# Kernel optimization log

Measured on AMD Instinct MI355X. Metric: run time of the kernel, lower is better.

Reference implementation:

```python
import jax, jax.numpy as jnp
import numpy as np

SLOTS, PER, EGO_D, PAIR_D, TER_D, TOK, HEADS, HDIM, VEC_H = 5, 15, 32, 10, 81, 32, 4, 8, 2


def layer_norm(x, s, b, eps=1e-6):
    mu = jnp.mean(x, axis=-1, keepdims=True)
    var = jnp.mean(jnp.square(x - mu), axis=-1, keepdims=True)
    return (x - mu) * jax.lax.rsqrt(var + eps) * s + b


def zero_masked(x, mask):
    while mask.ndim < x.ndim:
        mask = mask[..., None]
    return jnp.where(mask, x, 0.0)


def masked_softmax(logits, mask, axis):
    mask = mask.astype(jnp.bool_)
    while mask.ndim < logits.ndim:
        mask = mask[..., None]
    neg_big = jnp.finfo(logits.dtype).min
    has_any = jnp.any(mask, axis=axis, keepdims=True)
    ml = jnp.where(mask, logits, neg_big)
    ml = jnp.where(has_any, ml, 0.0)
    w = jax.nn.softmax(ml, axis=axis)
    w = jnp.where(mask, w, 0.0)
    denom = jnp.sum(w, axis=axis, keepdims=True)
    return jnp.where(denom > 0, w / denom, 0.0)


def _forward(x, w_ego, b_ego, w_pair, b_pair, w_ter, b_ter, w_invtok, b_invtok,
             tx_ln1_s, tx_ln1_b, tx_wq, tx_bq, tx_wk, tx_bk, tx_wv, tx_bv, tx_wo, tx_bo,
             tx_ln2_s, tx_ln2_b, tx_w1, tx_b1, tx_w2, tx_b2,
             sp_ln_s, sp_ln_b, sp_w, sp_b, sp_log_temp,
             ap_wq, ap_bq, ap_wk, ap_bk, ap_we, ap_be,
             flat_w, flat_b,
             vr_wego, vr_bego, vr_ln_s, vr_ln_b, vr_wh, vr_bh, vr_wl, vr_bl,
             z_w1, z_b1, z_ln1_s, z_ln1_b, z_w2, z_b2, z_ln2_s, z_ln2_b):
    gelu = jax.nn.gelu  # tanh-approximate, matching flax nn.gelu
    x = x.astype(jnp.float32)
    B, N, D = x.shape
    ego = x[..., :EGO_D]
    nbr = x[..., EGO_D:EGO_D + SLOTS * PER].reshape(B, N, SLOTS, PER)
    pair = x[..., EGO_D + SLOTS * PER:EGO_D + SLOTS * PER + PAIR_D]
    ter = x[..., -TER_D:]
    r = nbr[..., 0:3]; u = nbr[..., 3:6]; att_rel = nbr[..., 6:9]
    fire = nbr[..., 9:10]; teamdiff = nbr[..., 10:11]; inv4 = nbr[..., 11:15]
    mask = jnp.any(jnp.abs(r) > 1e-06, axis=-1)  # (B,N,K)
    att_norm = jnp.linalg.norm(att_rel, axis=-1, keepdims=True)
    ego_e = gelu(ego @ w_ego + b_ego)
    pair_e = gelu(pair @ w_pair + b_pair)
    ter_e = gelu(ter @ w_ter + b_ter)
    inv = jnp.concatenate([fire, teamdiff, inv4, att_rel, att_norm], axis=-1)
    inv = zero_masked(inv, mask)
    inv_tok = zero_masked(gelu(inv @ w_invtok + b_invtok), mask)  # (B,N,K,TOK)
    # --- SetTxBlock ---
    has_any = jnp.any(mask, axis=-1, keepdims=True)  # (B,N,1)
    fallback = (jnp.arange(SLOTS) == 0)
    mask_safe = jnp.where(has_any, mask, fallback)
    amask = mask_safe[..., :, None] & mask_safe[..., None, :]  # (B,N,Kq,Kk)
    t = inv_tok
    y = layer_norm(t, tx_ln1_s, tx_ln1_b)
    q = (y @ tx_wq + tx_bq).reshape(B, N, SLOTS, HEADS, HDIM)
    k = (y @ tx_wk + tx_bk).reshape(B, N, SLOTS, HEADS, HDIM)
    v = (y @ tx_wv + tx_bv).reshape(B, N, SLOTS, HEADS, HDIM)
    scores = jnp.einsum('bnqhd,bnkhd->bnhqk', q, k) / jnp.sqrt(jnp.float32(HDIM))
    scores = jnp.where(amask[:, :, None, :, :], scores, jnp.finfo(scores.dtype).min)
    attn = jax.nn.softmax(scores, axis=-1)
    y = jnp.einsum('bnhqk,bnkhd->bnqhd', attn, v).reshape(B, N, SLOTS, TOK)
    y = zero_masked(y @ tx_wo + tx_bo, mask)
    t = t + y
    y = layer_norm(t, tx_ln2_s, tx_ln2_b)
    y = gelu(y @ tx_w1 + tx_b1) @ tx_w2 + tx_b2
    t = zero_masked(t + zero_masked(y, mask), mask)
    inv_tok = t
    # --- pools ---
    inv_sum = jnp.sum(inv_tok, axis=-2)
    inv_cnt = jnp.maximum(jnp.sum(mask, axis=-1, keepdims=True), 1)
    inv_mean = inv_sum / inv_cnt
    inv_max = jnp.max(jnp.where(mask[..., None], inv_tok, -1e9), axis=-2)
    inv_max = jnp.where(has_any, inv_max, 0.0)
    # MaskedSoftmaxPool
    yln = layer_norm(inv_tok, sp_ln_s, sp_ln_b)
    sc = (yln @ sp_w + sp_b)[..., 0]
    temp = jax.nn.softplus(sp_log_temp) + 0.001
    wts = masked_softmax(temp * sc, mask, axis=-1)
    inv_soft = jnp.sum(wts[..., None] * inv_tok, axis=-2)
    # EgoAdditivePool
    qe = (ego_e @ ap_wq + ap_bq)[:, :, None, :]
    ke = inv_tok @ ap_wk + ap_bk
    e = (jnp.tanh(qe + ke) @ ap_we + ap_be)[..., 0]
    alpha = masked_softmax(e, mask, axis=-1)
    inv_add = jnp.sum(alpha[..., None] * inv_tok, axis=-2)
    # flat readout
    inv_flat = 0.25 * gelu(inv_tok.reshape(B, N, SLOTS * TOK) @ flat_w + flat_b)
    # InvariantVectorReadout
    ego_h = jnp.broadcast_to((ego_e @ vr_wego + vr_bego)[:, :, None, :], (B, N, SLOTS, TOK))
    h = jnp.concatenate([layer_norm(inv_tok, vr_ln_s, vr_ln_b), ego_h], axis=-1)
    h = gelu(h @ vr_wh + vr_bh)
    logits = h @ vr_wl + vr_bl  # (B,N,K,VEC_H)
    alpha2 = masked_softmax(logits, mask, axis=-2)
    v_r = jnp.einsum('bnkh,bnkd->bnhd', alpha2, r).reshape(B, N, 3 * VEC_H)
    v_u = jnp.einsum('bnkh,bnkd->bnhd', alpha2, u).reshape(B, N, 3 * VEC_H)
    z = jnp.concatenate([ego_e, pair_e, ter_e, inv_mean, inv_max, inv_soft, inv_add, inv_flat, v_r, v_u], axis=-1)
    z = layer_norm(gelu(z @ z_w1 + z_b1), z_ln1_s, z_ln1_b)
    z = layer_norm(gelu(z @ z_w2 + z_b2), z_ln2_s, z_ln2_b)
    return z


def setup_inputs() -> dict:
    key = jax.random.key(0)
    ks = iter(jax.random.split(key, 40))
    B, N = 64, 2048
    ego = jax.random.normal(next(ks), (B, N, EGO_D), jnp.float32)
    nbr = jax.random.normal(next(ks), (B, N, SLOTS, PER), jnp.float32)
    keep = jax.random.bernoulli(next(ks), 0.7, (B, N, SLOTS))
    nbr = nbr * keep[..., None]  # zeroed slots -> masked out (r == 0)
    pair = jax.random.normal(next(ks), (B, N, PAIR_D), jnp.float32)
    ter = jax.random.normal(next(ks), (B, N, TER_D), jnp.float32)
    x = jnp.concatenate([ego, nbr.reshape(B, N, SLOTS * PER), pair, ter], axis=-1)
    def W(i, o, s=0.05):
        return jax.random.normal(next(ks), (i, o), jnp.float32) * s
    Z = lambda *sh: jnp.zeros(sh, jnp.float32)
    O = lambda *sh: jnp.ones(sh, jnp.float32)
    Z_DIM = 64 + 32 + 64 + 4 * TOK + 32 + 12  # 332
    return dict(
        x=x,
        w_ego=W(EGO_D, 64), b_ego=Z(64), w_pair=W(PAIR_D, 32), b_pair=Z(32),
        w_ter=W(TER_D, 64), b_ter=Z(64), w_invtok=W(10, TOK), b_invtok=Z(TOK),
        tx_ln1_s=O(TOK), tx_ln1_b=Z(TOK),
        tx_wq=W(TOK, TOK), tx_bq=Z(TOK), tx_wk=W(TOK, TOK), tx_bk=Z(TOK),
        tx_wv=W(TOK, TOK), tx_bv=Z(TOK), tx_wo=W(TOK, TOK), tx_bo=Z(TOK),
        tx_ln2_s=O(TOK), tx_ln2_b=Z(TOK),
        tx_w1=W(TOK, 2 * TOK), tx_b1=Z(2 * TOK), tx_w2=W(2 * TOK, TOK), tx_b2=Z(TOK),
        sp_ln_s=O(TOK), sp_ln_b=Z(TOK), sp_w=W(TOK, 1), sp_b=Z(1), sp_log_temp=jnp.float32(0.0),
        ap_wq=W(64, TOK), ap_bq=Z(TOK), ap_wk=W(TOK, TOK), ap_bk=Z(TOK), ap_we=W(TOK, 1), ap_be=Z(1),
        flat_w=W(SLOTS * TOK, 32), flat_b=Z(32),
        vr_wego=W(64, TOK), vr_bego=Z(TOK), vr_ln_s=O(TOK), vr_ln_b=Z(TOK),
        vr_wh=W(2 * TOK, TOK), vr_bh=Z(TOK), vr_wl=W(TOK, VEC_H), vr_bl=Z(VEC_H),
        z_w1=W(Z_DIM, 128), z_b1=Z(128), z_ln1_s=O(128), z_ln1_b=Z(128),
        z_w2=W(128, 128), z_b2=Z(128), z_ln2_s=O(128), z_ln2_b=Z(128),
    )


def reference(x, w_ego, b_ego, w_pair, b_pair, w_ter, b_ter, w_invtok, b_invtok,
              tx_ln1_s, tx_ln1_b, tx_wq, tx_bq, tx_wk, tx_bk, tx_wv, tx_bv, tx_wo, tx_bo,
              tx_ln2_s, tx_ln2_b, tx_w1, tx_b1, tx_w2, tx_b2,
              sp_ln_s, sp_ln_b, sp_w, sp_b, sp_log_temp,
              ap_wq, ap_bq, ap_wk, ap_bk, ap_we, ap_be,
              flat_w, flat_b,
              vr_wego, vr_bego, vr_ln_s, vr_ln_b, vr_wh, vr_bh, vr_wl, vr_bl,
              z_w1, z_b1, z_ln1_s, z_ln1_b, z_w2, z_b2, z_ln2_s, z_ln2_b):
    return _forward(x, w_ego, b_ego, w_pair, b_pair, w_ter, b_ter, w_invtok, b_invtok,
                    tx_ln1_s, tx_ln1_b, tx_wq, tx_bq, tx_wk, tx_bk, tx_wv, tx_bv, tx_wo, tx_bo,
                    tx_ln2_s, tx_ln2_b, tx_w1, tx_b1, tx_w2, tx_b2,
                    sp_ln_s, sp_ln_b, sp_w, sp_b, sp_log_temp,
                    ap_wq, ap_bq, ap_wk, ap_bk, ap_we, ap_be,
                    flat_w, flat_b,
                    vr_wego, vr_bego, vr_ln_s, vr_ln_b, vr_wh, vr_bh, vr_wl, vr_bl,
                    z_w1, z_b1, z_ln1_s, z_ln1_b, z_w2, z_b2, z_ln2_s, z_ln2_b)
```

## Files before the change

kernel.cpp:

```cpp
#include <hip/hip_runtime.h>
#include <hip/hip_bf16.h>

#define SLOTS 5
#define PER 15
#define EGO_DD 32
#define PAIR_DD 10
#define TER_DD 81
#define DX 198
#define ZDIM 332
#define NTOK (64*2048)
#define NEGB (-3.402823466e38f)
#define ST 36
#define HBST 68
#define YHS 40
#define HHS 72

#define T_EGO   0
#define T_PAIR  4
#define T_TER   6
#define T_INV   18
#define T_Q     20
#define T_K     22
#define T_V     24
#define T_O     26
// ... 39 lines not shown
  __hip_bfloat16 h = __float2bfloat16(x);
  return *reinterpret_cast<short*>(&h);
}
__device__ __forceinline__ float tanh_f(float x){
  float e = __expf(2.f*x);
  return 1.f - 2.f/(e+1.f);
}
__device__ __forceinline__ float gelu_f(float x){
  return 0.5f*x*(1.f+tanh_f(0.7978845608028654f*(x + 0.044715f*x*x*x)));
}
__device__ __forceinline__ s16x8 packrow(const float* r){
  s16x8 af;
  #pragma unroll
  for(int j=0;j<8;j++) af[j]=f2bf(r[j]);
  return af;
}
__device__ __forceinline__ s16x8 packrowb(const float* r, int k0, int K){
  s16x8 af;
  #pragma unroll
  for(int j=0;j<8;j++) af[j] = (k0+j<K) ? f2bf(r[k0+j]) : (short)0;
  return af;
}

__device__ void msm5(const float* lgv, const int* m, float* outp, float scale){
  bool any = m[0]||m[1]||m[2]||m[3]||m[4];
  if(!any){ for(int s2=0;s2<5;s2++) outp[s2]=0.f; return; }
  float mx=NEGB;
  for(int s2=0;s2<5;s2++) if(m[s2]) mx=fmaxf(mx, scale*lgv[s2]);
  float e[5], se=0.f;
  for(int s2=0;s2<5;s2++){ e[s2]= m[s2]? __expf(scale*lgv[s2]-mx):0.f; se+=e[s2]; }
  float inv=1.f/se;
  for(int s2=0;s2<5;s2++) outp[s2]=e[s2]*inv;
}

__device__ void ln5x32(const float* src, float* dst, const float* Sc, const float* Bi, int l){
  for (int sp=0; sp<6; sp+=2){
    int sl = sp + (l>>5), i = l&31;
    bool act = sl < SLOTS;
    float v = act ? src[sl*ST+i] : 0.f;
    float sum=v;
    sum+=__shfl_xor(sum,16,32); sum+=__shfl_xor(sum,8,32); sum+=__shfl_xor(sum,4,32);
    sum+=__shfl_xor(sum,2,32);  sum+=__shfl_xor(sum,1,32);
    float mu=sum*(1.f/32.f);
    float d = v-mu;
    float q=d*d;
    q+=__shfl_xor(q,16,32); q+=__shfl_xor(q,8,32); q+=__shfl_xor(q,4,32);
    q+=__shfl_xor(q,2,32);  q+=__shfl_xor(q,1,32);
    float rstd=rsqrtf(q*(1.f/32.f)+1e-6f);
    if(act) dst[sl*ST+i]=d*rstd*Sc[i]+Bi[i];
  }
}
__device__ void ln5x32h(const float* src, short* dst, const float* Sc, const float* Bi, int l){
  for (int sp=0; sp<6; sp+=2){
    int sl = sp + (l>>5), i = l&31;
    bool act = sl < SLOTS;
    float v = act ? src[sl*ST+i] : 0.f;
    float sum=v;
    sum+=__shfl_xor(sum,16,32); sum+=__shfl_xor(sum,8,32); sum+=__shfl_xor(sum,4,32);
    sum+=__shfl_xor(sum,2,32);  sum+=__shfl_xor(sum,1,32);
    float mu=sum*(1.f/32.f);
    float d = v-mu;
    float q=d*d;
    q+=__shfl_xor(q,16,32); q+=__shfl_xor(q,8,32); q+=__shfl_xor(q,4,32);
    q+=__shfl_xor(q,2,32);  q+=__shfl_xor(q,1,32);
    float rstd=rsqrtf(q*(1.f/32.f)+1e-6f);
    if(act) dst[sl*YHS+i]=f2bf(d*rstd*Sc[i]+Bi[i]);
  }
}

__global__ __launch_bounds__(256) void k_prep(P p, short* __restrict__ ws){
  int idx = blockIdx.x*256 + threadIdx.x;
  if (idx >= T_TOT*512) return;
  int j = idx & 7, lane = (idx>>3)&63, tile = idx>>9;
  const float* src; int K,N,ntc,t0;
  if      (tile < T_PAIR){ src=p.w_ego;   K=32;  N=64;  ntc=4; t0=T_EGO; }
  else if (tile < T_TER ){ src=p.w_pair;  K=10;  N=32;  ntc=2; t0=T_PAIR; }
  else if (tile < T_INV ){ src=p.w_ter;   K=81;  N=64;  ntc=4; t0=T_TER; }
  else if (tile < T_Q   ){ src=p.w_invtok;K=10;  N=32;  ntc=2; t0=T_INV; }
  else if (tile < T_K   ){ src=p.wq;      K=32;  N=32;  ntc=2; t0=T_Q; }
  else if (tile < T_V   ){ src=p.wk;      K=32;  N=32;  ntc=2; t0=T_K; }
  else if (tile < T_O   ){ src=p.wv;      K=32;  N=32;  ntc=2; t0=T_V; }
  else if (tile < T_W1  ){ src=p.wo;      K=32;  N=32;  ntc=2; t0=T_O; }
  else if (tile < T_W2  ){ src=p.w1;      K=32;  N=64;  ntc=4; t0=T_W1; }
  else if (tile < T_APQ ){ src=p.w2;      K=64;  N=32;  ntc=2; t0=T_W2; }
  else if (tile < T_APK ){ src=p.ap_wq;   K=64;  N=32;  ntc=2; t0=T_APQ; }
  else if (tile < T_FLAT){ src=p.ap_wk;   K=32;  N=32;  ntc=2; t0=T_APK; }
  else if (tile < T_VEGO){ src=p.flat_w;  K=160; N=32;  ntc=2; t0=T_FLAT; }
  else if (tile < T_VH  ){ src=p.vr_wego; K=64;  N=32;  ntc=2; t0=T_VEGO; }
  else if (tile < T_ZW1 ){ src=p.vr_wh;   K=64;  N=32;  ntc=2; t0=T_VH; }
  else if (tile < T_ZW2 ){ src=p.z_w1;    K=ZDIM;N=128; ntc=8; t0=T_ZW1; }
  else                   { src=p.z_w2;    K=128; N=128; ntc=8; t0=T_ZW2; }
  int tl = tile - t0, ktI = tl/ntc, ntI = tl%ntc;
  int k = ktI*32 + ((lane>>4)<<3) + j, n = ntI*16 + (lane&15);
  float v = (k<K && n<N) ? src[k*N+n] : 0.f;
  ws[idx] = f2bf(v);
}

#define WV 4
__global__ __launch_bounds__(256) void k_token(P p, float* __restrict__ outp,
                                               const short* __restrict__ wsb) {
  __shared__ __align__(16) float pool[WV*PW];
  __shared__ int mkA[WV][5];
  __shared__ int mksA[WV][5];
  const s16x8* wsv = (const s16x8*)wsb;
  int wid = threadIdx.x >> 6, l = threadIdx.x & 63;
  float* W   = pool + wid*PW;
  float* ego = W + OF_EGO;
  float* tv  = W + OF_TV;
  float* yb  = W + OF_YB;
  short* ybh = (short*)(W + OF_YB);
  float* U   = W + OF_U;
  float* at  = W + OF_AT;
  float* zb  = W + OF_ZB;
  float* qeb = W + OF_QEB;
  float* egh = W + OF_EGH;
  float* ru  = W + OF_RU;
  float* sm  = W + OF_SM;
  float* scs = sm+0; float* wts = sm+5; float* alp = sm+10; float* lg = sm+16; float* a2 = sm+26;
  int* mk  = mkA[wid];
  int* mks = mksA[wid];
  float* xb = U;
  float* qb = U;  float* kb = U+180;  float* vb = U+360;
  float* hb = U;
  short* hbh = (short*)(U + 344);
  float* vq = U;
  long tok = (long)blockIdx.x*WV + wid;
  int m = l & 15, q = l >> 4;
  int mm = m < 5 ? m : 4;
#define BFR(tile) wsv[(tile)*64 + l]

  {
    const float2* xr2 = (const float2*)(p.x + (size_t)tok*DX);
    float2* xb2 = (float2*)xb;
    for (int i=l;i<99;i+=64) xb2[i] = xr2[i];
  }
  WF();

  if (l < SLOTS) { int nb = EGO_DD + l*PER;
    mk[l] = (fabsf(xb[nb])>1e-6f || fabsf(xb[nb+1])>1e-6f || fabsf(xb[nb+2])>1e-6f) ? 1 : 0; }
  if (l < 30){ int sl=l/6, d=l%6; ru[l] = xb[EGO_DD + sl*PER + d]; }
  WF();
  int nmask = mk[0]+mk[1]+mk[2]+mk[3]+mk[4];
  bool hasany = nmask>0;
  if (l < SLOTS) mks[l] = hasany ? mk[l] : (l==0 ? 1 : 0);

  {
    s16x8 aE = packrow(&xb[q*8]);
    s16x8 aP = packrowb(&xb[107], q*8, 10);
    f32x4 e0={0,0,0,0},e1={0,0,0,0},e2={0,0,0,0},e3={0,0,0,0};
    e0=MFMA(aE,BFR(T_EGO+0),e0); e1=MFMA(aE,BFR(T_EGO+1),e1);
    e2=MFMA(aE,BFR(T_EGO+2),e2); e3=MFMA(aE,BFR(T_EGO+3),e3);
    f32x4 p0={0,0,0,0},p1={0,0,0,0};
    p0=MFMA(aP,BFR(T_PAIR+0),p0); p1=MFMA(aP,BFR(T_PAIR+1),p1);
    if (l<16){
      zb[l]    = e0[0]+p.b_ego[l];    zb[16+l] = e1[0]+p.b_ego[16+l];
      zb[32+l] = e2[0]+p.b_ego[32+l]; zb[48+l] = e3[0]+p.b_ego[48+l];
      zb[64+l] = p0[0]+p.b_pair[l];   zb[80+l] = p1[0]+p.b_pair[16+l];
    }
  }
  {
    f32x4 t0={0,0,0,0},t1={0,0,0,0},t2={0,0,0,0},t3={0,0,0,0};
    for(int kt=0;kt<3;kt++){
      s16x8 aT = packrowb(&xb[117], kt*32+q*8, 81);
      t0=MFMA(aT,BFR(T_TER+kt*4+0),t0); t1=MFMA(aT,BFR(T_TER+kt*4+1),t1);
      t2=MFMA(aT,BFR(T_TER+kt*4+2),t2); t3=MFMA(aT,BFR(T_TER+kt*4+3),t3);
    }
    if (l<16){
      zb[96+l] = t0[0]+p.b_ter[l];    zb[112+l]= t1[0]+p.b_ter[16+l];
      zb[128+l]= t2[0]+p.b_ter[32+l]; zb[144+l]= t3[0]+p.b_ter[48+l];
    }
  }
  {
    int nb = EGO_DD + mm*PER;
    float a0=xb[nb+6],a1=xb[nb+7],a2v=xb[nb+8];
    float nrm = sqrtf(a0*a0+a1*a1+a2v*a2v);
    s16x8 af;
    #pragma unroll
    for(int j=0;j<8;j++){
      int k=q*8+j; float v;
      if(k<6) v=xb[nb+9+k];
      else if(k<9) v=xb[nb+k];
      else if(k==9) v=nrm;
      else v=0.f;
      af[j]=f2bf(v);
    }
    f32x4 c0={0,0,0,0},c1={0,0,0,0};
    c0=MFMA(af,BFR(T_INV+0),c0); c1=MFMA(af,BFR(T_INV+1),c1);
    #pragma unroll
    for(int r=0;r<4;r++){ int row=q*4+r;
      if(row<SLOTS){
        tv[row*ST+m]    = c0[r]+p.b_invtok[m];
        tv[row*ST+16+m] = c1[r]+p.b_invtok[16+m];
      }
    }
  }
  WF();
  if (l<40){
    f32x4 v = *(f32x4*)&zb[l*4];
    #pragma unroll
    for(int j=0;j<4;j++) v[j]=gelu_f(v[j]);
    *(f32x4*)&zb[l*4]=v;
    if (l<16) *(f32x4*)&ego[l*4]=v;
  }
  if (l<40){
    int sl=l>>3, i4=(l&7)*4;
    f32x4 v = *(f32x4*)&tv[sl*ST+i4];
    if (mk[sl]){
      #pragma unroll
      for(int j=0;j<4;j++) v[j]=gelu_f(v[j]);
    } else { v = (f32x4){0.f,0.f,0.f,0.f}; }
    *(f32x4*)&tv[sl*ST+i4]=v;
  }
  WF();

  ln5x32h(tv, ybh, p.ln1_s, p.ln1_b, l);
  WF();
  {
    s16x8 aY = *(const s16x8*)&ybh[mm*YHS + q*8];
    f32x4 q0={0,0,0,0},q1={0,0,0,0},k0v={0,0,0,0},k1v={0,0,0,0},v0={0,0,0,0},v1={0,0,0,0};
    q0=MFMA(aY,BFR(T_Q+0),q0);   q1=MFMA(aY,BFR(T_Q+1),q1);
    k0v=MFMA(aY,BFR(T_K+0),k0v); k1v=MFMA(aY,BFR(T_K+1),k1v);
    v0=MFMA(aY,BFR(T_V+0),v0);   v1=MFMA(aY,BFR(T_V+1),v1);
    #pragma unroll
    for(int r=0;r<4;r++){ int row=q*4+r;
      if(row<SLOTS){
        qb[row*ST+m]=q0[r]+p.bq[m];     qb[row*ST+16+m]=q1[r]+p.bq[16+m];
        kb[row*ST+m]=k0v[r]+p.bk[m];    kb[row*ST+16+m]=k1v[r]+p.bk[16+m];
        vb[row*ST+m]=v0[r]+p.bv[m];     vb[row*ST+16+m]=v1[r]+p.bv[16+m];
      }
    }
  }
  WF();
  for (int t=l; t<100; t+=64){
    int h=t/25, r2=t%25, qs=r2/5, ks=r2%5;
    const f32x4* qp=(const f32x4*)&qb[qs*ST+h*8];
    const f32x4* kp=(const f32x4*)&kb[ks*ST+h*8];
    f32x4 q0=qp[0], q1=qp[1], k0=kp[0], k1=kp[1];
    float d8 = q0[0]*k0[0]+q0[1]*k0[1]+q0[2]*k0[2]+q0[3]*k0[3]
             + q1[0]*k1[0]+q1[1]*k1[1]+q1[2]*k1[2]+q1[3]*k1[3];
    at[t] = (mks[qs]&&mks[ks]) ? d8*0.35355339059327373f : NEGB;
  }
  WF();
  if (l<20){
    float e[5]; float mx=NEGB, se=0.f;
    #pragma unroll
    for(int ks=0;ks<5;ks++) mx=fmaxf(mx, at[l*5+ks]);
    #pragma unroll
    for(int ks=0;ks<5;ks++){ e[ks]=__expf(at[l*5+ks]-mx); se+=e[ks]; }
    float inv=1.f/se;
    #pragma unroll
    for(int ks=0;ks<5;ks++) at[l*5+ks]=e[ks]*inv;
// ... 1 lines not shown
  WF();
  if (l<40){
    int sl=l>>3, i4=(l&7)*4, h=i4>>3, d=i4&7;
    f32x4 acc={0.f,0.f,0.f,0.f};
    #pragma unroll
    for(int ks=0;ks<5;ks++){
      float w = at[(h*5+sl)*5+ks];
      f32x4 vv = *(const f32x4*)&vb[ks*ST+h*8+d];
      acc += vv*w;
    }
    s16x4 o;
    #pragma unroll
    for(int j=0;j<4;j++) o[j]=f2bf(acc[j]);
    *(s16x4*)&ybh[sl*YHS+i4]=o;
  }
  WF();
  {
    s16x8 aY = *(const s16x8*)&ybh[mm*YHS + q*8];
    f32x4 c0={0,0,0,0},c1={0,0,0,0};
    c0=MFMA(aY,BFR(T_O+0),c0); c1=MFMA(aY,BFR(T_O+1),c1);
    #pragma unroll
    for(int r=0;r<4;r++){ int row=q*4+r;
      if(row<SLOTS && mk[row]){
        tv[row*ST+m]    += c0[r]+p.bo[m];
        tv[row*ST+16+m] += c1[r]+p.bo[16+m];
      }
    }
  }
  WF();
  ln5x32h(tv, ybh, p.ln2_s, p.ln2_b, l);
  WF();
  {
    s16x8 aY = *(const s16x8*)&ybh[mm*YHS + q*8];
    f32x4 c0={0,0,0,0},c1={0,0,0,0},c2={0,0,0,0},c3={0,0,0,0};
    c0=MFMA(aY,BFR(T_W1+0),c0); c1=MFMA(aY,BFR(T_W1+1),c1);
    c2=MFMA(aY,BFR(T_W1+2),c2); c3=MFMA(aY,BFR(T_W1+3),c3);
    #pragma unroll
    for(int r=0;r<4;r++){ int row=q*4+r;
      if(row<SLOTS){
        hb[row*HBST+m]   =c0[r]+p.b1[m];
        hb[row*HBST+16+m]=c1[r]+p.b1[16+m];
        hb[row*HBST+32+m]=c2[r]+p.b1[32+m];
        hb[row*HBST+48+m]=c3[r]+p.b1[48+m];
      }
    }
  }
  WF();
  for (int t=l;t<80;t+=64){
    int sl=t>>4, j4=(t&15)*4;
    f32x4 v = *(f32x4*)&hb[sl*HBST+j4];
    s16x4 o;
    #pragma unroll
    for(int j=0;j<4;j++) o[j]=f2bf(gelu_f(v[j]));
    *(s16x4*)&hbh[sl*HHS+j4]=o;
  }
  WF();
  {
    f32x4 c0={0,0,0,0},c1={0,0,0,0};
    for(int kt=0;kt<2;kt++){
      s16x8 aH = *(const s16x8*)&hbh[mm*HHS + kt*32 + q*8];
      c0=MFMA(aH,BFR(T_W2+kt*2+0),c0); c1=MFMA(aH,BFR(T_W2+kt*2+1),c1);
    }
    #pragma unroll
    for(int r=0;r<4;r++){ int row=q*4+r;
      if(row<SLOTS){
        float n0 = mk[row] ? tv[row*ST+m]+c0[r]+p.b2[m] : 0.f;
        float n1 = mk[row] ? tv[row*ST+16+m]+c1[r]+p.b2[16+m] : 0.f;
        tv[row*ST+m]=n0; tv[row*ST+16+m]=n1;
      }
    }
  }
  WF();

  if (l<32){
    float v0=tv[l],v1=tv[ST+l],v2=tv[2*ST+l],v3=tv[3*ST+l],v4=tv[4*ST+l];
    int cnt = nmask>0?nmask:1;
    zb[160+l]=(v0+v1+v2+v3+v4)/(float)cnt;
    float mx=-1e9f;
    if(mk[0])mx=fmaxf(mx,v0); if(mk[1])mx=fmaxf(mx,v1); if(mk[2])mx=fmaxf(mx,v2);
    if(mk[3])mx=fmaxf(mx,v3); if(mk[4])mx=fmaxf(mx,v4);
    zb[192+l]= hasany ? mx : 0.f;
  }
  ln5x32(tv, yb, p.sp_ln_s, p.sp_ln_b, l);
  WF();
  for (int sp=0; sp<6; sp+=2){
    int sl = sp + (l>>5), i = l&31;
    float v = (sl<SLOTS) ? yb[sl*ST+i]*p.sp_w[i] : 0.f;
    v+=__shfl_xor(v,16,32); v+=__shfl_xor(v,8,32); v+=__shfl_xor(v,4,32);
    v+=__shfl_xor(v,2,32);  v+=__shfl_xor(v,1,32);
    if (sl<SLOTS && i==0) scs[sl]=v+p.sp_b[0];
  }
  WF();
  if (l==0){
    float temp = log1pf(expf(p.sp_lt[0])) + 0.001f;
    msm5(scs, mk, wts, temp);
  }
  WF();
  if (l<32){ float a=0;
    for(int sl=0;sl<5;sl++) a += wts[sl]*tv[sl*ST+l];
    zb[224+l]=a; }
  {
    f32x4 c0={0,0,0,0},c1={0,0,0,0};
    for(int kt=0;kt<2;kt++){
      s16x8 aE = packrow(&ego[kt*32 + q*8]);
      c0=MFMA(aE,BFR(T_APQ+kt*2+0),c0); c1=MFMA(aE,BFR(T_APQ+kt*2+1),c1);
    }
    if(l<16){ qeb[l]=c0[0]+p.ap_bq[l]; qeb[16+l]=c1[0]+p.ap_bq[16+l]; }
  }
  WF();
  {
    s16x8 aT = packrow(&tv[mm*ST + q*8]);
    f32x4 c0={0,0,0,0},c1={0,0,0,0};
    c0=MFMA(aT,BFR(T_APK+0),c0); c1=MFMA(aT,BFR(T_APK+1),c1);
    #pragma unroll
    for(int r=0;r<4;r++){ int row=q*4+r;
      if(row<SLOTS){
        yb[row*ST+m]   =c0[r]+p.ap_bk[m]+qeb[m];
        yb[row*ST+16+m]=c1[r]+p.ap_bk[16+m]+qeb[16+m];
      }
    }
  }
  WF();
  if (l<40){
    int sl=l>>3, i4=(l&7)*4;
    f32x4 v = *(f32x4*)&yb[sl*ST+i4];
    #pragma unroll
    for(int j=0;j<4;j++) v[j]=tanh_f(v[j]);
    *(f32x4*)&yb[sl*ST+i4]=v;
  }
  WF();
  for (int sp=0; sp<6; sp+=2){
    int sl = sp + (l>>5), i = l&31;
    float v = (sl<SLOTS) ? yb[sl*ST+i]*p.ap_we[i] : 0.f;
    v+=__shfl_xor(v,16,32); v+=__shfl_xor(v,8,32); v+=__shfl_xor(v,4,32);
    v+=__shfl_xor(v,2,32);  v+=__shfl_xor(v,1,32);
    if (sl<SLOTS && i==0) scs[sl]=v+p.ap_be[0];
  }
  WF();
  if (l==0) msm5(scs, mk, alp, 1.f);
  WF();
  if (l<32){ float a=0;
    for(int sl=0;sl<5;sl++) a += alp[sl]*tv[sl*ST+l];
    zb[256+l]=a; }
  {
    f32x4 c0={0,0,0,0},c1={0,0,0,0};
    for(int kt=0;kt<5;kt++){
      s16x8 aF = packrow(&tv[kt*ST + q*8]);
      c0=MFMA(aF,BFR(T_FLAT+kt*2+0),c0); c1=MFMA(aF,BFR(T_FLAT+kt*2+1),c1);
    }
    if(l<16){ zb[288+l]=c0[0]+p.flat_b[l]; zb[304+l]=c1[0]+p.flat_b[16+l]; }
  }
  {
    f32x4 c0={0,0,0,0},c1={0,0,0,0};
    for(int kt=0;kt<2;kt++){
      s16x8 aE = packrow(&ego[kt*32 + q*8]);
      c0=MFMA(aE,BFR(T_VEGO+kt*2+0),c0); c1=MFMA(aE,BFR(T_VEGO+kt*2+1),c1);
    }
    if(l<16){ egh[l]=c0[0]+p.vr_bego[l]; egh[16+l]=c1[0]+p.vr_bego[16+l]; }
  }
  WF();
  if(l<32) zb[288+l]=0.25f*gelu_f(zb[288+l]);
  ln5x32h(tv, ybh, p.vr_ln_s, p.vr_ln_b, l);
  WF();
  {
    s16x8 aY = *(const s16x8*)&ybh[mm*YHS + q*8];
    s16x8 aE = packrow(&egh[q*8]);
    f32x4 c0={0,0,0,0},c1={0,0,0,0};
    c0=MFMA(aY,BFR(T_VH+0),c0); c1=MFMA(aY,BFR(T_VH+1),c1);
    c0=MFMA(aE,BFR(T_VH+2),c0); c1=MFMA(aE,BFR(T_VH+3),c1);
    #pragma unroll
    for(int r=0;r<4;r++){ int row=q*4+r;
      if(row<SLOTS){
        vq[row*ST+m]   =c0[r]+p.vr_bh[m];
        vq[row*ST+16+m]=c1[r]+p.vr_bh[16+m];
      }
    }
  }
  WF();
  if (l<40){
    int sl=l>>3, i4=(l&7)*4;
    f32x4 v = *(f32x4*)&vq[sl*ST+i4];
    #pragma unroll
    for(int j=0;j<4;j++) v[j]=gelu_f(v[j]);
    *(f32x4*)&vq[sl*ST+i4]=v;
  }
  WF();
  for (int t=0; t<5; t++){
    int idx = t*2 + (l>>5);
    int sl = idx>>1, hh = idx&1, i = l&31;
    float v = vq[sl*ST+i]*p.vr_wl[i*2+hh];
    v+=__shfl_xor(v,16,32); v+=__shfl_xor(v,8,32); v+=__shfl_xor(v,4,32);
    v+=__shfl_xor(v,2,32);  v+=__shfl_xor(v,1,32);
    if (i==0) lg[idx]=v+p.vr_bl[hh];
  }
  WF();
  if (l<2){ float tmp[5],o5[5];
    for(int sl=0;sl<5;sl++) tmp[sl]=lg[sl*2+l];
    msm5(tmp, mk, o5, 1.f);
    for(int sl=0;sl<5;sl++) a2[sl*2+l]=o5[sl]; }
  WF();
  if (l<12){ int w = l/6, rem=l%6, hh=rem/3, d=rem%3;
    float a=0;
    for(int sl=0;sl<5;sl++) a += a2[sl*2+hh]*ru[sl*6 + w*3 + d];
    zb[320 + w*6 + hh*3 + d]=a; }
  WF();

  {
    short* zbh = (short*)(W + OF_U + 300);
    for (int t=l;t<88;t+=64){
      s16x4 o;
      if (t<83){
        f32x4 v = *(const f32x4*)&zb[t*4];
        #pragma unroll
        for(int j=0;j<4;j++) o[j]=f2bf(v[j]);
      } else {
        #pragma unroll
        for(int j=0;j<4;j++) o[j]=0;
      }
      *(s16x4*)&zbh[t*4]=o;
    }
  }
  __syncthreads();

  {
    f32x4 acc0 = {0.f,0.f,0.f,0.f}, acc1 = {0.f,0.f,0.f,0.f};
    const short* zbhM = (const short*)(pool + (m<4?m:0)*PW + OF_U + 300);
    for (int kt=0; kt<11; kt++){
      s16x8 af;
      if (m < 4) af = *(const s16x8*)&zbhM[kt*32 + q*8];
      else {
        #pragma unroll
        for (int j=0;j<8;j++) af[j]=0;
      }
      s16x8 b0 = wsv[(T_ZW1 + kt*8 + 2*wid  )*64 + l];
      s16x8 b1 = wsv[(T_ZW1 + kt*8 + 2*wid+1)*64 + l];
      acc0 = MFMA(af, b0, acc0);
      acc1 = MFMA(af, b1, acc1);
    }
    if (q == 0){
      int c0 = 2*wid*16 + m, c1 = (2*wid+1)*16 + m;
      float bb0 = p.z_b1[c0], bb1 = p.z_b1[c1];
      #pragma unroll
      for (int r=0;r<4;r++){
        pool[r*PW + OF_U + c0] = gelu_f(acc0[r] + bb0);
        pool[r*PW + OF_U + c1] = gelu_f(acc1[r] + bb1);
      }
    }
  }
  __syncthreads();
  {
    float v0 = pool[wid*PW + OF_U + l], v1 = pool[wid*PW + OF_U + l+64];
    float sum = v0+v1;
    for (int o=32;o>=1;o>>=1) sum += __shfl_xor(sum,o,64);
    float mu = sum*(1.f/128.f);
    float d0=v0-mu, d1=v1-mu;
    float qq = d0*d0+d1*d1;
    for (int o=32;o>=1;o>>=1) qq += __shfl_xor(qq,o,64);
    float rs = rsqrtf(qq*(1.f/128.f)+1e-6f);
    short* h1h = (short*)(W + OF_U + 476);
    h1h[l]    = f2bf(d0*rs*p.z_ln1_s[l]   +p.z_ln1_b[l]);
    h1h[l+64] = f2bf(d1*rs*p.z_ln1_s[l+64]+p.z_ln1_b[l+64]);
  }
  __syncthreads();
  {
    f32x4 acc0 = {0.f,0.f,0.f,0.f}, acc1 = {0.f,0.f,0.f,0.f};
    const short* h1hM = (const short*)(pool + (m<4?m:0)*PW + OF_U + 476);
    for (int kt=0; kt<4; kt++){
      s16x8 af;
      if (m < 4) af = *(const s16x8*)&h1hM[kt*32 + q*8];
      else {
        #pragma unroll
        for (int j=0;j<8;j++) af[j]=0;
      }
      s16x8 b0 = wsv[(T_ZW2 + kt*8 + 2*wid  )*64 + l];
      s16x8 b1 = wsv[(T_ZW2 + kt*8 + 2*wid+1)*64 + l];
      acc0 = MFMA(af, b0, acc0);
      acc1 = MFMA(af, b1, acc1);
    }
    if (q == 0){
      int c0 = 2*wid*16 + m, c1 = (2*wid+1)*16 + m;
      float bb0 = p.z_b2[c0], bb1 = p.z_b2[c1];
      #pragma unroll
      for (int r=0;r<4;r++){
        pool[r*PW + OF_U + 128 + c0] = gelu_f(acc0[r] + bb0);
        pool[r*PW + OF_U + 128 + c1] = gelu_f(acc1[r] + bb1);
      }
    }
  }
  __syncthreads();
  {
    float v0 = pool[wid*PW + OF_U + 128 + l], v1 = pool[wid*PW + OF_U + 128 + l+64];
    float sum = v0+v1;
    for (int o=32;o>=1;o>>=1) sum += __shfl_xor(sum,o,64);
    float mu = sum*(1.f/128.f);
    float d0=v0-mu, d1=v1-mu;
    float qq = d0*d0+d1*d1;
    for (int o=32;o>=1;o>>=1) qq += __shfl_xor(qq,o,64);
    float rs = rsqrtf(qq*(1.f/128.f)+1e-6f);
    float o0 = d0*rs*p.z_ln2_s[l]   +p.z_ln2_b[l];
    float o1 = d1*rs*p.z_ln2_s[l+64]+p.z_ln2_b[l+64];
    float* op = outp + (size_t)tok*128;
    op[l]    = o0;
    op[l+64] = o1;
  }
}

extern "C" void kernel_launch(void* const* d_in, const int* in_sizes, int n_in,
                              void* d_out, int out_size, void* d_ws, size_t ws_size,
                              hipStream_t stream) {
  (void)in_sizes; (void)n_in; (void)out_size; (void)ws_size;
  P p;
  const void** pp = (const void**)&p;
  for (int i=0;i<54;i++) pp[i] = d_in[i];
  short* wsb = (short*)d_ws;
  k_prep<<<(T_TOT*512+255)/256, 256, 0, stream>>>(p, wsb);
  k_token<<<NTOK/WV, 256, 0, stream>>>(p, (float*)d_out, wsb);
}
```

Baseline: 1.249 ms.

## Restructure pooling tail: hoist params to registers, fuse layernorms, parallelize softmaxes

```diff
diff --git a/kernel.cpp b/kernel.cpp
--- a/kernel.cpp
+++ b/kernel.cpp
@@ -85,49 +85,46 @@
   return af;
 }
 
-__device__ void msm5(const float* lgv, const int* m, float* outp, float scale){
-  bool any = m[0]||m[1]||m[2]||m[3]||m[4];
-  if(!any){ for(int s2=0;s2<5;s2++) outp[s2]=0.f; return; }
-  float mx=NEGB;
-  for(int s2=0;s2<5;s2++) if(m[s2]) mx=fmaxf(mx, scale*lgv[s2]);
-  float e[5], se=0.f;
-  for(int s2=0;s2<5;s2++){ e[s2]= m[s2]? __expf(scale*lgv[s2]-mx):0.f; se+=e[s2]; }
-  float inv=1.f/se;
-  for(int s2=0;s2<5;s2++) outp[s2]=e[s2]*inv;
-}
-
-__device__ void ln5x32(const float* src, float* dst, const float* Sc, const float* Bi, int l){
+__device__ __forceinline__ void red5_2(float&a,float&b){
+  a+=__shfl_xor(a,16,32); b+=__shfl_xor(b,16,32);
+  a+=__shfl_xor(a,8,32);  b+=__shfl_xor(b,8,32);
+  a+=__shfl_xor(a,4,32);  b+=__shfl_xor(b,4,32);
+  a+=__shfl_xor(a,2,32);  b+=__shfl_xor(b,2,32);
+  a+=__shfl_xor(a,1,32);  b+=__shfl_xor(b,1,32);
+}
+__device__ __forceinline__ float red5(float a){
+  a+=__shfl_xor(a,16,32); a+=__shfl_xor(a,8,32); a+=__shfl_xor(a,4,32);
+  a+=__shfl_xor(a,2,32);  a+=__shfl_xor(a,1,32);
+  return a;
+}
+
+__device__ void ln5h(const float* src, short* dst, float sc, float bi, int l){
   for (int sp=0; sp<6; sp+=2){
     int sl = sp + (l>>5), i = l&31;
     bool act = sl < SLOTS;
     float v = act ? src[sl*ST+i] : 0.f;
-    float sum=v;
-    sum+=__shfl_xor(sum,16,32); sum+=__shfl_xor(sum,8,32); sum+=__shfl_xor(sum,4,32);
-    sum+=__shfl_xor(sum,2,32);  sum+=__shfl_xor(sum,1,32);
-    float mu=sum*(1.f/32.f);
-    float d = v-mu;
-    float q=d*d;
-    q+=__shfl_xor(q,16,32); q+=__shfl_xor(q,8,32); q+=__shfl_xor(q,4,32);
-    q+=__shfl_xor(q,2,32);  q+=__shfl_xor(q,1,32);
-    float rstd=rsqrtf(q*(1.f/32.f)+1e-6f);
-    if(act) dst[sl*ST+i]=d*rstd*Sc[i]+Bi[i];
-  }
-}
-__device__ void ln5x32h(const float* src, short* dst, const float* Sc, const float* Bi, int l){
+    float s=v, ss=v*v;
+    red5_2(s,ss);
+    float mu=s*(1.f/32.f);
+    float rstd=rsqrtf(ss*(1.f/32.f)-mu*mu+1e-6f);
+    if(act) dst[sl*YHS+i]=f2bf((v-mu)*rstd*sc+bi);
+  }
+}
+__device__ void ln5_spvr(const float* src, short* ath, float* scs,
+    float s_sp,float b_sp,float s_vr,float b_vr,float w_sp,float spb,int l){
   for (int sp=0; sp<6; sp+=2){
     int sl = sp + (l>>5), i = l&31;
     bool act = sl < SLOTS;
     float v = act ? src[sl*ST+i] : 0.f;
-    float sum=v;
-    sum+=__shfl_xor(sum,16,32); sum+=__shfl_xor(sum,8,32); sum+=__shfl_xor(sum,4,32);
-    sum+=__shfl_xor(sum,2,32);  sum+=__shfl_xor(sum,1,32);
-    float mu=sum*(1.f/32.f);
-    float d = v-mu;
-    float q=d*d;
-    q+=__shfl_xor(q,16,32); q+=__shfl_xor(q,8,32); q+=__shfl_xor(q,4,32);
-    q+=__shfl_xor(q,2,32);  q+=__shfl_xor(q,1,32);
-    float rstd=rsqrtf(q*(1.f/32.f)+1e-6f);
-    if(act) dst[sl*YHS+i]=f2bf(d*rstd*Sc[i]+Bi[i]);
+    float s=v, ss=v*v;
+    red5_2(s,ss);
+    float mu=s*(1.f/32.f);
+    float rstd=rsqrtf(ss*(1.f/32.f)-mu*mu+1e-6f);
+    float d=(v-mu)*rstd;
+    if(act) ath[sl*YHS+i]=f2bf(d*s_vr+b_vr);
+    float t=(d*s_sp+b_sp)*w_sp;
+    t=red5(t);
+    if(act && i==0) scs[sl]=t+spb;
   }
 }
 
@@ -174,12 +171,14 @@
   short* ybh = (short*)(W + OF_YB);
   float* U   = W + OF_U;
   float* at  = W + OF_AT;
+  short* ath = (short*)(W + OF_AT);
   float* zb  = W + OF_ZB;
   float* qeb = W + OF_QEB;
   float* egh = W + OF_EGH;
   float* ru  = W + OF_RU;
   float* sm  = W + OF_SM;
-  float* scs = sm+0; float* wts = sm+5; float* alp = sm+10; float* lg = sm+16; float* a2 = sm+26;
+  float* scs = sm+0; float* wts = sm+5; float* alp = sm+10; float* lg = sm+16;
+  float* a2 = sm+26; float* aps = sm+36;
   int* mk  = mkA[wid];
   int* mks = mksA[wid];
   float* xb = U;
@@ -190,7 +189,43 @@
   long tok = (long)blockIdx.x*WV + wid;
   int m = l & 15, q = l >> 4;
   int mm = m < 5 ? m : 4;
+  int i5 = l & 31, l16 = l & 15;
 #define BFR(tile) wsv[(tile)*64 + l]
+
+  float r_binv0=p.b_invtok[m],  r_binv1=p.b_invtok[16+m];
+  float r_bq0=p.bq[m], r_bq1=p.bq[16+m];
+  float r_bk0=p.bk[m], r_bk1=p.bk[16+m];
+  float r_bv0=p.bv[m], r_bv1=p.bv[16+m];
+  float r_bo0=p.bo[m], r_bo1=p.bo[16+m];
+  float r_b10=p.b1[m], r_b11=p.b1[16+m], r_b12=p.b1[32+m], r_b13=p.b1[48+m];
+  float r_b20=p.b2[m], r_b21=p.b2[16+m];
+  float r_vbh0=p.vr_bh[m], r_vbh1=p.vr_bh[16+m];
+  float r_bego0=p.b_ego[l16], r_bego1=p.b_ego[16+l16],
+        r_bego2=p.b_ego[32+l16], r_bego3=p.b_ego[48+l16];
+  float r_bpair0=p.b_pair[l16], r_bpair1=p.b_pair[16+l16];
+  float r_bter0=p.b_ter[l16], r_bter1=p.b_ter[16+l16],
+        r_bter2=p.b_ter[32+l16], r_bter3=p.b_ter[48+l16];
+  float r_apbq0=p.ap_bq[l16], r_apbq1=p.ap_bq[16+l16];
+  float r_fb0=p.flat_b[l16], r_fb1=p.flat_b[16+l16];
+  float r_vbe0=p.vr_bego[l16], r_vbe1=p.vr_bego[16+l16];
+  float r_ln1s=p.ln1_s[i5], r_ln1b=p.ln1_b[i5];
+  float r_ln2s=p.ln2_s[i5], r_ln2b=p.ln2_b[i5];
+  float r_spls=p.sp_ln_s[i5], r_splb=p.sp_ln_b[i5];
+  float r_vrls=p.vr_ln_s[i5], r_vrlb=p.vr_ln_b[i5];
+  float r_spw=p.sp_w[i5];
+  float r_apwe=p.ap_we[i5];
+  float r_apbki=p.ap_bk[i5];
+  float r_vwl0=p.vr_wl[i5*2], r_vwl1=p.vr_wl[i5*2+1];
+  float r_spb=p.sp_b[0], r_apbe=p.ap_be[0];
+  float r_vbl0=p.vr_bl[0], r_vbl1=p.vr_bl[1];
+  float r_spt = log1pf(expf(p.sp_lt[0])) + 0.001f;
+  int   zc0 = 2*wid*16 + m, zc1 = (2*wid+1)*16 + m;
+  float r_zb1c0=p.z_b1[zc0], r_zb1c1=p.z_b1[zc1];
+  float r_zb2c0=p.z_b2[zc0], r_zb2c1=p.z_b2[zc1];
+  float r_zl1s0=p.z_ln1_s[l], r_zl1s1=p.z_ln1_s[l+64];
+  float r_zl1b0=p.z_ln1_b[l], r_zl1b1=p.z_ln1_b[l+64];
+  float r_zl2s0=p.z_ln2_s[l], r_zl2s1=p.z_ln2_s[l+64];
+  float r_zl2b0=p.z_ln2_b[l], r_zl2b1=p.z_ln2_b[l+64];
 
   {
     const float2* xr2 = (const float2*)(p.x + (size_t)tok*DX);
@@ -202,10 +237,6 @@
   if (l < SLOTS) { int nb = EGO_DD + l*PER;
     mk[l] = (fabsf(xb[nb])>1e-6f || fabsf(xb[nb+1])>1e-6f || fabsf(xb[nb+2])>1e-6f) ? 1 : 0; }
   if (l < 30){ int sl=l/6, d=l%6; ru[l] = xb[EGO_DD + sl*PER + d]; }
-  WF();
-  int nmask = mk[0]+mk[1]+mk[2]+mk[3]+mk[4];
-  bool hasany = nmask>0;
-  if (l < SLOTS) mks[l] = hasany ? mk[l] : (l==0 ? 1 : 0);
 
   {
     s16x8 aE = packrow(&xb[q*8]);
@@ -216,9 +247,9 @@
     f32x4 p0={0,0,0,0},p1={0,0,0,0};
     p0=MFMA(aP,BFR(T_PAIR+0),p0); p1=MFMA(aP,BFR(T_PAIR+1),p1);
     if (l<16){
-      zb[l]    = e0[0]+p.b_ego[l];    zb[16+l] = e1[0]+p.b_ego[16+l];
-      zb[32+l] = e2[0]+p.b_ego[32+l]; zb[48+l] = e3[0]+p.b_ego[48+l];
-      zb[64+l] = p0[0]+p.b_pair[l];   zb[80+l] = p1[0]+p.b_pair[16+l];
+      zb[l]    = e0[0]+r_bego0;   zb[16+l] = e1[0]+r_bego1;
+      zb[32+l] = e2[0]+r_bego2;   zb[48+l] = e3[0]+r_bego3;
+      zb[64+l] = p0[0]+r_bpair0;  zb[80+l] = p1[0]+r_bpair1;
     }
   }
   {
@@ -229,8 +260,8 @@
       t2=MFMA(aT,BFR(T_TER+kt*4+2),t2); t3=MFMA(aT,BFR(T_TER+kt*4+3),t3);
     }
     if (l<16){
-      zb[96+l] = t0[0]+p.b_ter[l];    zb[112+l]= t1[0]+p.b_ter[16+l];
-      zb[128+l]= t2[0]+p.b_ter[32+l]; zb[144+l]= t3[0]+p.b_ter[48+l];
+      zb[96+l] = t0[0]+r_bter0;   zb[112+l]= t1[0]+r_bter1;
+      zb[128+l]= t2[0]+r_bter2;   zb[144+l]= t3[0]+r_bter3;
     }
   }
   {
@@ -252,12 +283,15 @@
     #pragma unroll
     for(int r=0;r<4;r++){ int row=q*4+r;
       if(row<SLOTS){
-        tv[row*ST+m]    = c0[r]+p.b_invtok[m];
-        tv[row*ST+16+m] = c1[r]+p.b_invtok[16+m];
-      }
-    }
-  }
-  WF();
+        tv[row*ST+m]    = c0[r]+r_binv0;
+        tv[row*ST+16+m] = c1[r]+r_binv1;
+      }
+    }
+  }
+  WF();
+  int nmask = mk[0]+mk[1]+mk[2]+mk[3]+mk[4];
+  bool hasany = nmask>0;
+  if (l < SLOTS) mks[l] = hasany ? mk[l] : (l==0 ? 1 : 0);
   if (l<40){
     f32x4 v = *(f32x4*)&zb[l*4];
     #pragma unroll
@@ -276,7 +310,7 @@
   }
   WF();
 
-  ln5x32h(tv, ybh, p.ln1_s, p.ln1_b, l);
+  ln5h(tv, ybh, r_ln1s, r_ln1b, l);
   WF();
   {
     s16x8 aY = *(const s16x8*)&ybh[mm*YHS + q*8];
@@ -287,9 +321,9 @@
     #pragma unroll
     for(int r=0;r<4;r++){ int row=q*4+r;
       if(row<SLOTS){
-        qb[row*ST+m]=q0[r]+p.bq[m];     qb[row*ST+16+m]=q1[r]+p.bq[16+m];
-        kb[row*ST+m]=k0v[r]+p.bk[m];    kb[row*ST+16+m]=k1v[r]+p.bk[16+m];
-        vb[row*ST+m]=v0[r]+p.bv[m];     vb[row*ST+16+m]=v1[r]+p.bv[16+m];
+        qb[row*ST+m]=q0[r]+r_bq0;     qb[row*ST+16+m]=q1[r]+r_bq1;
+        kb[row*ST+m]=k0v[r]+r_bk0;    kb[row*ST+16+m]=k1v[r]+r_bk1;
+        vb[row*ST+m]=v0[r]+r_bv0;     vb[row*ST+16+m]=v1[r]+r_bv1;
       }
     }
   }
@@ -337,13 +371,13 @@
     #pragma unroll
     for(int r=0;r<4;r++){ int row=q*4+r;
       if(row<SLOTS && mk[row]){
-        tv[row*ST+m]    += c0[r]+p.bo[m];
-        tv[row*ST+16+m] += c1[r]+p.bo[16+m];
-      }
-    }
-  }
-  WF();
-  ln5x32h(tv, ybh, p.ln2_s, p.ln2_b, l);
+        tv[row*ST+m]    += c0[r]+r_bo0;
+        tv[row*ST+16+m] += c1[r]+r_bo1;
+      }
+    }
+  }
+  WF();
+  ln5h(tv, ybh, r_ln2s, r_ln2b, l);
   WF();
   {
     s16x8 aY = *(const s16x8*)&ybh[mm*YHS + q*8];
@@ -353,10 +387,10 @@
     #pragma unroll
     for(int r=0;r<4;r++){ int row=q*4+r;
       if(row<SLOTS){
-        hb[row*HBST+m]   =c0[r]+p.b1[m];
-        hb[row*HBST+16+m]=c1[r]+p.b1[16+m];
-        hb[row*HBST+32+m]=c2[r]+p.b1[32+m];
-        hb[row*HBST+48+m]=c3[r]+p.b1[48+m];
+        hb[row*HBST+m]   =c0[r]+r_b10;
+        hb[row*HBST+16+m]=c1[r]+r_b11;
+        hb[row*HBST+32+m]=c2[r]+r_b12;
+        hb[row*HBST+48+m]=c3[r]+r_b13;
       }
     }
   }
@@ -379,14 +413,46 @@
     #pragma unroll
     for(int r=0;r<4;r++){ int row=q*4+r;
       if(row<SLOTS){
-        float n0 = mk[row] ? tv[row*ST+m]+c0[r]+p.b2[m] : 0.f;
-        float n1 = mk[row] ? tv[row*ST+16+m]+c1[r]+p.b2[16+m] : 0.f;
+        float n0 = mk[row] ? tv[row*ST+m]+c0[r]+r_b20 : 0.f;
+        float n1 = mk[row] ? tv[row*ST+16+m]+c1[r]+r_b21 : 0.f;
         tv[row*ST+m]=n0; tv[row*ST+16+m]=n1;
       }
     }
   }
   WF();
 
+  {
+    f32x4 c0={0,0,0,0},c1={0,0,0,0},d0={0,0,0,0},d1={0,0,0,0};
+    for(int kt=0;kt<2;kt++){
+      s16x8 aE = packrow(&ego[kt*32 + q*8]);
+      c0=MFMA(aE,BFR(T_APQ+kt*2+0),c0); c1=MFMA(aE,BFR(T_APQ+kt*2+1),c1);
+      d0=MFMA(aE,BFR(T_VEGO+kt*2+0),d0); d1=MFMA(aE,BFR(T_VEGO+kt*2+1),d1);
+    }
+    if(l<16){
+      qeb[l]=c0[0]+r_apbq0; qeb[16+l]=c1[0]+r_apbq1;
+      egh[l]=d0[0]+r_vbe0;  egh[16+l]=d1[0]+r_vbe1;
+    }
+  }
+  {
+    f32x4 c0={0,0,0,0},c1={0,0,0,0};
+    for(int kt=0;kt<5;kt++){
+      s16x8 aF = packrow(&tv[kt*ST + q*8]);
+      c0=MFMA(aF,BFR(T_FLAT+kt*2+0),c0); c1=MFMA(aF,BFR(T_FLAT+kt*2+1),c1);
+    }
+    if(l<16){ zb[288+l]=c0[0]+r_fb0; zb[304+l]=c1[0]+r_fb1; }
+  }
+  {
+    s16x8 aT = packrow(&tv[mm*ST + q*8]);
+    f32x4 c0={0,0,0,0},c1={0,0,0,0};
+    c0=MFMA(aT,BFR(T_APK+0),c0); c1=MFMA(aT,BFR(T_APK+1),c1);
+    #pragma unroll
+    for(int r=0;r<4;r++){ int row=q*4+r;
+      if(row<SLOTS){
+        yb[row*ST+m]   =c0[r];
+        yb[row*ST+16+m]=c1[r];
+      }
+    }
+  }
   if (l<32){
     float v0=tv[l],v1=tv[ST+l],v2=tv[2*ST+l],v3=tv[3*ST+l],v4=tv[4*ST+l];
     int cnt = nmask>0?nmask:1;
@@ -396,89 +462,28 @@
     if(mk[3])mx=fmaxf(mx,v3); if(mk[4])mx=fmaxf(mx,v4);
     zb[192+l]= hasany ? mx : 0.f;
   }
-  ln5x32(tv, yb, p.sp_ln_s, p.sp_ln_b, l);
-  WF();
+  ln5_spvr(tv, ath, scs, r_spls, r_splb, r_vrls, r_vrlb, r_spw, r_spb, l);
+  WF();
+
+  if (l<8){
+    bool keep=(l<5)&&(mk[l]!=0);
+    float x= keep? r_spt*scs[l] : NEGB;
+    float mx=x;
+    mx=fmaxf(mx,__shfl_xor(mx,1,8)); mx=fmaxf(mx,__shfl_xor(mx,2,8)); mx=fmaxf(mx,__shfl_xor(mx,4,8));
+    float e= keep? __expf(x-mx):0.f;
+    float se=e;
+    se+=__shfl_xor(se,1,8); se+=__shfl_xor(se,2,8); se+=__shfl_xor(se,4,8);
+    if (l<5) wts[l]= se>0.f? e/se:0.f;
+  }
+  if(l<32) zb[288+l]=0.25f*gelu_f(zb[288+l]);
   for (int sp=0; sp<6; sp+=2){
     int sl = sp + (l>>5), i = l&31;
-    float v = (sl<SLOTS) ? yb[sl*ST+i]*p.sp_w[i] : 0.f;
-    v+=__shfl_xor(v,16,32); v+=__shfl_xor(v,8,32); v+=__shfl_xor(v,4,32);
-    v+=__shfl_xor(v,2,32);  v+=__shfl_xor(v,1,32);
-    if (sl<SLOTS && i==0) scs[sl]=v+p.sp_b[0];
-  }
-  WF();
-  if (l==0){
-    float temp = log1pf(expf(p.sp_lt[0])) + 0.001f;
-    msm5(scs, mk, wts, temp);
-  }
-  WF();
-  if (l<32){ float a=0;
-    for(int sl=0;sl<5;sl++) a += wts[sl]*tv[sl*ST+l];
-    zb[224+l]=a; }
-  {
-    f32x4 c0={0,0,0,0},c1={0,0,0,0};
-    for(int kt=0;kt<2;kt++){
-      s16x8 aE = packrow(&ego[kt*32 + q*8]);
-      c0=MFMA(aE,BFR(T_APQ+kt*2+0),c0); c1=MFMA(aE,BFR(T_APQ+kt*2+1),c1);
-    }
-    if(l<16){ qeb[l]=c0[0]+p.ap_bq[l]; qeb[16+l]=c1[0]+p.ap_bq[16+l]; }
-  }
-  WF();
-  {
-    s16x8 aT = packrow(&tv[mm*ST + q*8]);
-    f32x4 c0={0,0,0,0},c1={0,0,0,0};
-    c0=MFMA(aT,BFR(T_APK+0),c0); c1=MFMA(aT,BFR(T_APK+1),c1);
-    #pragma unroll
-    for(int r=0;r<4;r++){ int row=q*4+r;
-      if(row<SLOTS){
-        yb[row*ST+m]   =c0[r]+p.ap_bk[m]+qeb[m];
-        yb[row*ST+16+m]=c1[r]+p.ap_bk[16+m]+qeb[16+m];
-      }
-    }
-  }
-  WF();
-  if (l<40){
-    int sl=l>>3, i4=(l&7)*4;
-    f32x4 v = *(f32x4*)&yb[sl*ST+i4];
-    #pragma unroll
-    for(int j=0;j<4;j++) v[j]=tanh_f(v[j]);
-    *(f32x4*)&yb[sl*ST+i4]=v;
-  }
-  WF();
-  for (int sp=0; sp<6; sp+=2){
-    int sl = sp + (l>>5), i = l&31;
-    float v = (sl<SLOTS) ? yb[sl*ST+i]*p.ap_we[i] : 0.f;
-    v+=__shfl_xor(v,16,32); v+=__shfl_xor(v,8,32); v+=__shfl_xor(v,4,32);
-    v+=__shfl_xor(v,2,32);  v+=__shfl_xor(v,1,32);
-    if (sl<SLOTS && i==0) scs[sl]=v+p.ap_be[0];
-  }
-  WF();
-  if (l==0) msm5(scs, mk, alp, 1.f);
-  WF();
-  if (l<32){ float a=0;
-    for(int sl=0;sl<5;sl++) a += alp[sl]*tv[sl*ST+l];
-    zb[256+l]=a; }
-  {
-    f32x4 c0={0,0,0,0},c1={0,0,0,0};
-    for(int kt=0;kt<5;kt++){
-      s16x8 aF = packrow(&tv[kt*ST + q*8]);
-      c0=MFMA(aF,BFR(T_FLAT+kt*2+0),c0); c1=MFMA(aF,BFR(T_FLAT+kt*2+1),c1);
-    }
-    if(l<16){ zb[288+l]=c0[0]+p.flat_b[l]; zb[304+l]=c1[0]+p.flat_b[16+l]; }
-  }
-  {
-    f32x4 c0={0,0,0,0},c1={0,0,0,0};
-    for(int kt=0;kt<2;kt++){
-      s16x8 aE = packrow(&ego[kt*32 + q*8]);
-      c0=MFMA(aE,BFR(T_VEGO+kt*2+0),c0); c1=MFMA(aE,BFR(T_VEGO+kt*2+1),c1);
-    }
-    if(l<16){ egh[l]=c0[0]+p.vr_bego[l]; egh[16+l]=c1[0]+p.vr_bego[16+l]; }
-  }
-  WF();
-  if(l<32) zb[288+l]=0.25f*gelu_f(zb[288+l]);
-  ln5x32h(tv, ybh, p.vr_ln_s, p.vr_ln_b, l);
-  WF();
-  {
-    s16x8 aY = *(const s16x8*)&ybh[mm*YHS + q*8];
+    float v = (sl<SLOTS) ? tanh_f(yb[sl*ST+i]+r_apbki+qeb[i])*r_apwe : 0.f;
+    v=red5(v);
+    if (sl<SLOTS && i==0) aps[sl]=v+r_apbe;
+  }
+  {
+    s16x8 aY = *(const s16x8*)&ath[mm*YHS + q*8];
     s16x8 aE = packrow(&egh[q*8]);
     f32x4 c0={0,0,0,0},c1={0,0,0,0};
     c0=MFMA(aY,BFR(T_VH+0),c0); c1=MFMA(aY,BFR(T_VH+1),c1);
@@ -486,34 +491,51 @@
     #pragma unroll
     for(int r=0;r<4;r++){ int row=q*4+r;
       if(row<SLOTS){
-        vq[row*ST+m]   =c0[r]+p.vr_bh[m];
-        vq[row*ST+16+m]=c1[r]+p.vr_bh[16+m];
-      }
-    }
-  }
-  WF();
-  if (l<40){
-    int sl=l>>3, i4=(l&7)*4;
-    f32x4 v = *(f32x4*)&vq[sl*ST+i4];
-    #pragma unroll
-    for(int j=0;j<4;j++) v[j]=gelu_f(v[j]);
-    *(f32x4*)&vq[sl*ST+i4]=v;
-  }
-  WF();
+        vq[row*ST+m]   =c0[r]+r_vbh0;
+        vq[row*ST+16+m]=c1[r]+r_vbh1;
+      }
+    }
+  }
+  WF();
+
+  if (l<32){ float a=0;
+    for(int sl=0;sl<5;sl++) a += wts[sl]*tv[sl*ST+l];
+    zb[224+l]=a; }
+  if (l<8){
+    bool keep=(l<5)&&(mk[l]!=0);
+    float x= keep? aps[l] : NEGB;
+    float mx=x;
+    mx=fmaxf(mx,__shfl_xor(mx,1,8)); mx=fmaxf(mx,__shfl_xor(mx,2,8)); mx=fmaxf(mx,__shfl_xor(mx,4,8));
+    float e= keep? __expf(x-mx):0.f;
+    float se=e;
+    se+=__shfl_xor(se,1,8); se+=__shfl_xor(se,2,8); se+=__shfl_xor(se,4,8);
+    if (l<5) alp[l]= se>0.f? e/se:0.f;
+  }
   for (int t=0; t<5; t++){
-    int idx = t*2 + (l>>5);
-    int sl = idx>>1, hh = idx&1, i = l&31;
-    float v = vq[sl*ST+i]*p.vr_wl[i*2+hh];
-    v+=__shfl_xor(v,16,32); v+=__shfl_xor(v,8,32); v+=__shfl_xor(v,4,32);
-    v+=__shfl_xor(v,2,32);  v+=__shfl_xor(v,1,32);
-    if (i==0) lg[idx]=v+p.vr_bl[hh];
-  }
-  WF();
-  if (l<2){ float tmp[5],o5[5];
-    for(int sl=0;sl<5;sl++) tmp[sl]=lg[sl*2+l];
-    msm5(tmp, mk, o5, 1.f);
-    for(int sl=0;sl<5;sl++) a2[sl*2+l]=o5[sl]; }
-  WF();
+    int hh = l>>5, sl = t, i = l&31;
+    float g = gelu_f(vq[sl*ST+i]);
+    float v = g*(hh? r_vwl1 : r_vwl0);
+    v=red5(v);
+    if (i==0) lg[sl*2+hh]=v+(hh? r_vbl1 : r_vbl0);
+  }
+  WF();
+
+  if (l<32){ float a=0;
+    for(int sl=0;sl<5;sl++) a += alp[sl]*tv[sl*ST+l];
+    zb[256+l]=a; }
+  if (l<16){
+    int s=l&7, hh=l>>3;
+    bool keep=(s<5)&&(mk[s<5?s:0]!=0);
+    float x= keep? lg[(s<5?s:0)*2+hh] : NEGB;
+    float mx=x;
+    mx=fmaxf(mx,__shfl_xor(mx,1,8)); mx=fmaxf(mx,__shfl_xor(mx,2,8)); mx=fmaxf(mx,__shfl_xor(mx,4,8));
+    float e= keep? __expf(x-mx):0.f;
+    float se=e;
+    se+=__shfl_xor(se,1,8); se+=__shfl_xor(se,2,8); se+=__shfl_xor(se,4,8);
+    if (s<5) a2[s*2+hh]= se>0.f? e/se:0.f;
+  }
+  WF();
+
   if (l<12){ int w = l/6, rem=l%6, hh=rem/3, d=rem%3;
     float a=0;
     for(int sl=0;sl<5;sl++) a += a2[sl*2+hh]*ru[sl*6 + w*3 + d];
@@ -553,28 +575,23 @@
       acc1 = MFMA(af, b1, acc1);
     }
     if (q == 0){
-      int c0 = 2*wid*16 + m, c1 = (2*wid+1)*16 + m;
-      float bb0 = p.z_b1[c0], bb1 = p.z_b1[c1];
       #pragma unroll
       for (int r=0;r<4;r++){
-        pool[r*PW + OF_U + c0] = gelu_f(acc0[r] + bb0);
-        pool[r*PW + OF_U + c1] = gelu_f(acc1[r] + bb1);
+        pool[r*PW + OF_U + zc0] = gelu_f(acc0[r] + r_zb1c0);
+        pool[r*PW + OF_U + zc1] = gelu_f(acc1[r] + r_zb1c1);
       }
     }
   }
   __syncthreads();
   {
     float v0 = pool[wid*PW + OF_U + l], v1 = pool[wid*PW + OF_U + l+64];
-    float sum = v0+v1;
-    for (int o=32;o>=1;o>>=1) sum += __shfl_xor(sum,o,64);
+    float sum = v0+v1, qq = v0*v0+v1*v1;
+    for (int o=32;o>=1;o>>=1){ sum += __shfl_xor(sum,o,64); qq += __shfl_xor(qq,o,64); }
     float mu = sum*(1.f/128.f);
-    float d0=v0-mu, d1=v1-mu;
-    float qq = d0*d0+d1*d1;
-    for (int o=32;o>=1;o>>=1) qq += __shfl_xor(qq,o,64);
-    float rs = rsqrtf(qq*(1.f/128.f)+1e-6f);
+    float rs = rsqrtf(qq*(1.f/128.f)-mu*mu+1e-6f);
     short* h1h = (short*)(W + OF_U + 476);
-    h1h[l]    = f2bf(d0*rs*p.z_ln1_s[l]   +p.z_ln1_b[l]);
-    h1h[l+64] = f2bf(d1*rs*p.z_ln1_s[l+64]+p.z_ln1_b[l+64]);
+    h1h[l]    = f2bf((v0-mu)*rs*r_zl1s0+r_zl1b0);
+    h1h[l+64] = f2bf((v1-mu)*rs*r_zl1s1+r_zl1b1);
   }
   __syncthreads();
   {
@@ -593,27 +610,22 @@
       acc1 = MFMA(af, b1, acc1);
     }
     if (q == 0){
-      int c0 = 2*wid*16 + m, c1 = (2*wid+1)*16 + m;
-      float bb0 = p.z_b2[c0], bb1 = p.z_b2[c1];
       #pragma unroll
       for (int r=0;r<4;r++){
-        pool[r*PW + OF_U + 128 + c0] = gelu_f(acc0[r] + bb0);
-        pool[r*PW + OF_U + 128 + c1] = gelu_f(acc1[r] + bb1);
+        pool[r*PW + OF_U + 128 + zc0] = gelu_f(acc0[r] + r_zb2c0);
+        pool[r*PW + OF_U + 128 + zc1] = gelu_f(acc1[r] + r_zb2c1);
       }
     }
   }
   __syncthreads();
   {
     float v0 = pool[wid*PW + OF_U + 128 + l], v1 = pool[wid*PW + OF_U + 128 + l+64];
-    float sum = v0+v1;
-    for (int o=32;o>=1;o>>=1) sum += __shfl_xor(sum,o,64);
+    float sum = v0+v1, qq = v0*v0+v1*v1;
+    for (int o=32;o>=1;o>>=1){ sum += __shfl_xor(sum,o,64); qq += __shfl_xor(qq,o,64); }
     float mu = sum*(1.f/128.f);
-    float d0=v0-mu, d1=v1-mu;
-    float qq = d0*d0+d1*d1;
-    for (int o=32;o>=1;o>>=1) qq += __shfl_xor(qq,o,64);
-    float rs = rsqrtf(qq*(1.f/128.f)+1e-6f);
-    float o0 = d0*rs*p.z_ln2_s[l]   +p.z_ln2_b[l];
-    float o1 = d1*rs*p.z_ln2_s[l+64]+p.z_ln2_b[l+64];
+    float rs = rsqrtf(qq*(1.f/128.f)-mu*mu+1e-6f);
+    float o0 = (v0-mu)*rs*r_zl2s0+r_zl2b0;
+    float o1 = (v1-mu)*rs*r_zl2s1+r_zl2b1;
     float* op = outp + (size_t)tok*128;
     op[l]    = o0;
     op[l+64] = o1;
```

New measurement: 1.642 ms. 31.5% more time.
